# Kernel tuning notes

Measured on AMD Instinct MI355X. Metric: run time of the kernel, lower is better.

Reference implementation:

```python
import jax, jax.numpy as jnp
import numpy as np

N = 50000      # nodes
E = 800000     # edges (before self-loops)
F_IN = 128     # nfeat
H = 4          # heads
C = 64         # GAT out_channels per head
HID = 128      # GCN hidden
NCLASS = 10
NEG = 0.2      # leaky-relu negative slope (alpha)


def setup_inputs() -> dict:
    key = jax.random.key(0)
    ks = jax.random.split(key, 10)
    init = lambda k, shape, fan: jax.random.normal(k, shape, jnp.float32) / np.sqrt(fan).astype(np.float32)
    return {
        "x": jax.random.normal(ks[0], (N, F_IN), jnp.float32),
        "edge_attr": jax.random.normal(ks[1], (E, 8), jnp.float32),  # ignored (edge_dim=None in GATConv)
        "Wg": init(ks[2], (F_IN, H * C), F_IN),
        "att_src": init(ks[3], (H, C), C),
        "att_dst": init(ks[4], (H, C), C),
        "bg": jnp.zeros((H * C,), jnp.float32),
        "Wc": init(ks[5], (H * C, HID), H * C),
        "bc": jnp.zeros((HID,), jnp.float32),
        "Wl": init(ks[6], (HID, NCLASS), HID),
        "bl": jnp.zeros((NCLASS,), jnp.float32),
        "edge_index": jax.random.randint(ks[7], (2, E), 0, N, dtype=jnp.int64),
    }


def reference(x, edge_attr, Wg, att_src, att_dst, bg, Wc, bc, Wl, bl, edge_index):
    del edge_attr  # GATConv with edge_dim=None ignores edge_attr
    loop = jnp.arange(N, dtype=edge_index.dtype)
    src = jnp.concatenate([edge_index[0], loop])  # message sources j (add_self_loops=True)
    dst = jnp.concatenate([edge_index[1], loop])  # message targets i

    # ---- GATConv (concat=True) ----
    h = (x @ Wg).reshape(N, H, C)                     # [N,H,C]
    a_s = jnp.einsum('nhc,hc->nh', h, att_src)        # [N,H]
    a_d = jnp.einsum('nhc,hc->nh', h, att_dst)
    e = a_s[src] + a_d[dst]                           # [E2,H]
    e = jnp.where(e > 0, e, NEG * e)                  # leaky_relu
    m = jax.ops.segment_max(e, dst, num_segments=N)   # segment softmax over incoming edges
    ex = jnp.exp(e - m[dst])
    denom = jax.ops.segment_sum(ex, dst, num_segments=N)
    alpha = ex / denom[dst]                           # [E2,H]
    agg = jax.ops.segment_sum(alpha[:, :, None] * h[src], dst, num_segments=N)  # [N,H,C]
    xg = jax.nn.elu(agg.reshape(N, H * C) + bg)

    # ---- GCNConv (sym-normalized SpMM with self-loops) ----
    deg = jax.ops.segment_sum(jnp.ones_like(dst, dtype=jnp.float32), dst, num_segments=N)
    dinv = jnp.where(deg > 0, 1.0 / jnp.sqrt(deg), 0.0)
    norm = dinv[src] * dinv[dst]                      # [E2]
    xw = xg @ Wc                                      # [N,HID]
    xc = jax.ops.segment_sum(norm[:, None] * xw[src], dst, num_segments=N) + bc
    xc = jax.nn.relu(xc)

    # ---- classifier head ----
    logits = xc @ Wl + bl                             # [N,NCLASS]
    return jax.nn.log_softmax(logits, axis=1)
```

## Files before the change

kernel.cpp:

```cpp
#include <hip/hip_runtime.h>
#include <hip/hip_fp16.h>
#include <math.h>

#define NN 50000
#define EE 800000
#define E2 (EE + NN)
#define FIN 128
#define HC 256
#define HID 128
#define NCLS 10
#define NEG 0.2f
#define NB2 196
#define NBLK 256
#define WPART ((E2 + NBLK - 1) / NBLK)

typedef _Float16 f16x8 __attribute__((ext_vector_type(8)));
typedef float f32x4 __attribute__((ext_vector_type(4)));

#define FMA_MIX_LO(acc, u, w) \
    asm("v_fma_mix_f32 %0, %1, %2, %0 op_sel:[0,0,0] op_sel_hi:[1,0,0]" \
        : "+v"(acc) : "v"(u), "v"(w))
#define FMA_MIX_HI(acc, u, w) \
    asm("v_fma_mix_f32 %0, %1, %2, %0 op_sel:[1,0,0] op_sel_hi:[1,0,0]" \
        : "+v"(acc) : "v"(u), "v"(w))

__device__ inline uint pack2h(float a, float b) {
    return (uint)__half_as_ushort(__float2half(a)) |
           ((uint)__half_as_ushort(__float2half(b)) << 16);
}

__global__ __launch_bounds__(256) void prep_kernel(const float* __restrict__ Wg,
                                                   const float* __restrict__ Wc,
                                                   const float* __restrict__ att_s,
                                                   const float* __restrict__ att_d,
                                                   ushort* __restrict__ wgt,
                                                   ushort* __restrict__ wct,
                                                   float4* __restrict__ vs,
                                                   float4* __restrict__ vd) {
    int i = blockIdx.x * 256 + threadIdx.x;
    if (i < HC * FIN) {
        int c = i & 255, k = i >> 8;
        wgt[c * FIN + k] = __half_as_ushort(__float2half(Wg[i]));
        int c2 = i & 127, k2 = i >> 7;
        wct[c2 * HC + k2] = __half_as_ushort(__float2half(Wc[i]));
    }
    if (blockIdx.x == 0 && threadIdx.x < FIN) {
        int k = threadIdx.x;
        float s[4] = {0.f, 0.f, 0.f, 0.f}, d[4] = {0.f, 0.f, 0.f, 0.f};
        for (int h = 0; h < 4; ++h)
            for (int c = 0; c < 64; ++c) {
                float wv = Wg[k * HC + h * 64 + c];
                s[h] += wv * att_s[h * 64 + c];
                d[h] += wv * att_d[h * 64 + c];
            }
        vs[k] = make_float4(s[0], s[1], s[2], s[3]);
        vd[k] = make_float4(d[0], d[1], d[2], d[3]);
    }
}

__global__ __launch_bounds__(256) void prep_x(const float* __restrict__ x,
                                              const float4* __restrict__ vs,
                                              const float4* __restrict__ vd,
                                              ushort* __restrict__ x_half,
                                              float* __restrict__ a_s,
                                              float* __restrict__ a_d) {
    const int node = blockIdx.x * 4 + (threadIdx.x >> 6);
    const int lane = threadIdx.x & 63;
    if (node >= NN) return;
    float2 xv = ((const float2*)(x + (size_t)node * FIN))[lane];
    ((uint*)x_half)[(size_t)node * 64 + lane] = pack2h(xv.x, xv.y);
    float4 v0 = vs[2 * lane], v1 = vs[2 * lane + 1];
    float4 d0 = vd[2 * lane], d1 = vd[2 * lane + 1];
    float ps0 = xv.x * v0.x + xv.y * v1.x;
    float ps1 = xv.x * v0.y + xv.y * v1.y;
    float ps2 = xv.x * v0.z + xv.y * v1.z;
    float ps3 = xv.x * v0.w + xv.y * v1.w;
    float pd0 = xv.x * d0.x + xv.y * d1.x;
    float pd1 = xv.x * d0.y + xv.y * d1.y;
    float pd2 = xv.x * d0.z + xv.y * d1.z;
    float pd3 = xv.x * d0.w + xv.y * d1.w;
#pragma unroll
    for (int m = 32; m >= 1; m >>= 1) {
        ps0 += __shfl_xor(ps0, m, 64); ps1 += __shfl_xor(ps1, m, 64);
        ps2 += __shfl_xor(ps2, m, 64); ps3 += __shfl_xor(ps3, m, 64);
        pd0 += __shfl_xor(pd0, m, 64); pd1 += __shfl_xor(pd1, m, 64);
        pd2 += __shfl_xor(pd2, m, 64); pd3 += __shfl_xor(pd3, m, 64);
    }
    if (lane == 0) {
        ((float4*)a_s)[node] = make_float4(ps0, ps1, ps2, ps3);
        ((float4*)a_d)[node] = make_float4(pd0, pd1, pd2, pd3);
    }
}

__global__ __launch_bounds__(256) void hist_coarse(const int* __restrict__ ei,
                                                   uint* __restrict__ blockhist) {
    __shared__ uint h[NB2];
    for (int i = threadIdx.x; i < NB2; i += 256) h[i] = 0;
    __syncthreads();
    int e0 = blockIdx.x * WPART, e1 = min(E2, e0 + WPART);
    for (int e = e0 + threadIdx.x; e < e1; e += 256) {
        int dst = (e < EE) ? ei[EE + e] : e - EE;
        atomicAdd(&h[dst >> 8], 1u);
    }
    __syncthreads();
    for (int i = threadIdx.x; i < NB2; i += 256) blockhist[i * NBLK + blockIdx.x] = h[i];
}

__global__ __launch_bounds__(256) void scan_blocks(const uint* __restrict__ blockhist,
                                                   uint* __restrict__ blockoff,
                                                   uint* __restrict__ total) {
    __shared__ uint sh[256];
    int b = blockIdx.x, t = threadIdx.x;
    uint v = blockhist[b * NBLK + t];
    sh[t] = v;
    __syncthreads();
#pragma unroll
    for (int off = 1; off < 256; off <<= 1) {
        uint y = (t >= off) ? sh[t - off] : 0;
        __syncthreads();
        sh[t] += y;
        __syncthreads();
    }
    blockoff[b * NBLK + t] = sh[t] - v;
    if (t == 255) total[b] = sh[255];
}

__global__ __launch_bounds__(256) void scan_buckets(const uint* __restrict__ total,
                                                    uint* __restrict__ bucket_base) {
    __shared__ uint sh[256];
    int t = threadIdx.x;
    uint v = (t < NB2) ? total[t] : 0;
    sh[t] = v;
    __syncthreads();
#pragma unroll
    for (int off = 1; off < 256; off <<= 1) {
        uint y = (t >= off) ? sh[t - off] : 0;
        __syncthreads();
        sh[t] += y;
        __syncthreads();
    }
    if (t < NB2) bucket_base[t] = sh[t] - v;
    if (t == NB2 - 1) bucket_base[NB2] = sh[t];
}

__global__ __launch_bounds__(256) void reorder_kernel(const int* __restrict__ ei,
                                                      const uint* __restrict__ blockoff,
                                                      const uint* __restrict__ bucket_base,
                                                      uint* __restrict__ ebuf) {
    __shared__ uint cur[NB2];
    for (int i = threadIdx.x; i < NB2; i += 256)
        cur[i] = bucket_base[i] + blockoff[i * NBLK + blockIdx.x];
    __syncthreads();
    int e0 = blockIdx.x * WPART, e1 = min(E2, e0 + WPART);
    for (int e = e0 + threadIdx.x; e < e1; e += 256) {
        int src, dst;
        if (e < EE) { src = ei[e]; dst = ei[EE + e]; }
        else        { src = dst = e - EE; }
        uint p = atomicAdd(&cur[dst >> 8], 1u);
        ebuf[p] = (uint)src | ((uint)(dst & 255) << 16);
    }
}

__global__ __launch_bounds__(256) void bucket_csr(const uint* __restrict__ ebuf,
                                                  const uint* __restrict__ bucket_base,
                                                  int* __restrict__ row_start,
                                                  float* __restrict__ dinv,
                                                  ushort* __restrict__ csr_src) {
    __shared__ uint ldeg[256], lcur[256], sh[256];
    const int b = blockIdx.x, t = threadIdx.x;
    const uint base = bucket_base[b], end = bucket_base[b + 1];
    ldeg[t] = 0;
    __syncthreads();
    for (uint i = base + t; i < end; i += 256) atomicAdd(&ldeg[ebuf[i] >> 16], 1u);
    __syncthreads();
    uint v = ldeg[t];
    sh[t] = v;
    __syncthreads();
#pragma unroll
    for (int off = 1; off < 256; off <<= 1) {
        uint y = (t >= off) ? sh[t - off] : 0;
        __syncthreads();
        sh[t] += y;
        __syncthreads();
    }
    uint lscan = sh[t] - v;
    int node = b * 256 + t;
    if (node < NN) {
        row_start[node] = (int)(base + lscan);
        dinv[node] = rsqrtf((float)v);
    }
    lcur[t] = base + lscan;
    __syncthreads();
    for (uint i = base + t; i < end; i += 256) {
        uint pk = ebuf[i];
        uint p = atomicAdd(&lcur[pk >> 16], 1u);
        csr_src[p] = (ushort)(pk & 0xFFFFu);
    }
    if (b == 0 && t == 0) row_start[NN] = E2;
}

__global__ __launch_bounds__(256) void gat_x(const ushort* __restrict__ x_half,
                                             const float* __restrict__ a_s,
                                             const float* __restrict__ a_d,
                                             const int* __restrict__ row_start,
                                             const ushort* __restrict__ csr_src,
                                             ushort* __restrict__ y) {
    __shared__ int    lds_off[4][64];
    __shared__ float4 lds_ex[4][64];
    const int wid  = threadIdx.x >> 6;
    const int lane = threadIdx.x & 63;
    const int node = blockIdx.x * 4 + wid;
    if (node >= NN) return;
    const int s0 = row_start[node], s1 = row_start[node + 1];
    const float4 ad = ((const float4*)a_d)[node];

    float den0 = 0.f, den1 = 0.f, den2 = 0.f, den3 = 0.f;
    float a00=0.f,a01=0.f,a10=0.f,a11=0.f,a20=0.f,a21=0.f,a30=0.f,a31=0.f;
    const char* xbase = (const char*)x_half;
    const uint lane4 = (uint)lane * 4;

#define GAT_BODY(J)                                                \
    {                                                              \
        int off = lds_off[wid][J];                                 \
        float4 ex = lds_ex[wid][J];                                \
        uint u = *(const uint*)(xbase + ((uint)off + lane4));      \
        FMA_MIX_LO(a00, u, ex.x); FMA_MIX_HI(a01, u, ex.x);        \
        FMA_MIX_LO(a10, u, ex.y); FMA_MIX_HI(a11, u, ex.y);        \
        FMA_MIX_LO(a20, u, ex.z); FMA_MIX_HI(a21, u, ex.z);        \
        FMA_MIX_LO(a30, u, ex.w); FMA_MIX_HI(a31, u, ex.w);        \
    }

    for (int e = s0; e < s1; e += 64) {
        const int m = min(64, s1 - e);
        if (lane < m) {
            int src = (int)csr_src[e + lane];
            float4 as = ((const float4*)a_s)[src];
            float v0 = as.x + ad.x; v0 = v0 > 0.f ? v0 : NEG * v0;
            float v1 = as.y + ad.y; v1 = v1 > 0.f ? v1 : NEG * v1;
            float v2 = as.z + ad.z; v2 = v2 > 0.f ? v2 : NEG * v2;
            float v3 = as.w + ad.w; v3 = v3 > 0.f ? v3 : NEG * v3;
            float e0 = __expf(v0); den0 += e0;
            float e1 = __expf(v1); den1 += e1;
            float e2 = __expf(v2); den2 += e2;
            float e3 = __expf(v3); den3 += e3;
            lds_off[wid][lane] = src * 256;
            lds_ex[wid][lane]  = make_float4(e0, e1, e2, e3);
        }
        asm volatile("s_waitcnt lgkmcnt(0)" ::: "memory");
        int j = 0;
        for (; j + 8 <= m; j += 8) {
            GAT_BODY(j);     GAT_BODY(j + 1); GAT_BODY(j + 2); GAT_BODY(j + 3);
            GAT_BODY(j + 4); GAT_BODY(j + 5); GAT_BODY(j + 6); GAT_BODY(j + 7);
        }
        for (; j < m; ++j) GAT_BODY(j);
        asm volatile("" ::: "memory");
    }
#undef GAT_BODY
#pragma unroll
    for (int m = 32; m >= 1; m >>= 1) {
        den0 += __shfl_xor(den0, m, 64);
        den1 += __shfl_xor(den1, m, 64);
        den2 += __shfl_xor(den2, m, 64);
        den3 += __shfl_xor(den3, m, 64);
    }
    float r0 = 1.f / den0, r1 = 1.f / den1, r2 = 1.f / den2, r3 = 1.f / den3;
    uint* yrow = (uint*)y + (size_t)node * 256;
    yrow[0 * 64 + lane] = pack2h(a00 * r0, a01 * r0);
    yrow[1 * 64 + lane] = pack2h(a10 * r1, a11 * r1);
    yrow[2 * 64 + lane] = pack2h(a20 * r2, a21 * r2);
    yrow[3 * 64 + lane] = pack2h(a30 * r3, a31 * r3);
}

__global__ __launch_bounds__(256) void proj_mfma(const ushort* __restrict__ y,
                                                 const ushort* __restrict__ wgt,
                                                 const float* __restrict__ bg,
                                                 ushort* __restrict__ xg) {
    __shared__ ushort hs[16][264];
    const int t = threadIdx.x;
    const int w  = t >> 6;
    const int l  = t & 63;
    const int lr = l & 15;
    const int lg = l >> 4;
    const int rr = t >> 4;
    const int rc = (t & 15) * 8;

    f16x8 bf[4][4];
#pragma unroll
    for (int ct = 0; ct < 4; ++ct)
#pragma unroll
        for (int ks = 0; ks < 4; ++ks)
            bf[ct][ks] = *(const f16x8*)(wgt + (size_t)(64 * w + 16 * ct + lr) * FIN + ks * 32 + 8 * lg);

    float bgv[4];
#pragma unroll
    for (int ct = 0; ct < 4; ++ct) bgv[ct] = bg[64 * w + 16 * ct + lr];

    for (int rt = blockIdx.x; rt < 3125; rt += gridDim.x) {
        const int r0 = rt * 16;
        f32x4 acc[4];
#pragma unroll
        for (int ct = 0; ct < 4; ++ct) acc[ct] = (f32x4){0.f, 0.f, 0.f, 0.f};

#pragma unroll
        for (int ks = 0; ks < 4; ++ks) {
            f16x8 af = *(const f16x8*)(y + (size_t)(r0 + lr) * 512 + w * 128 + ks * 32 + 8 * lg);
#pragma unroll
            for (int ct = 0; ct < 4; ++ct)
                acc[ct] = __builtin_amdgcn_mfma_f32_16x16x32_f16(af, bf[ct][ks], acc[ct], 0, 0, 0);
        }
#pragma unroll
        for (int j = 0; j < 4; ++j) {
#pragma unroll
            for (int ct = 0; ct < 4; ++ct) {
                float o = acc[ct][j] + bgv[ct];
                o = o > 0.f ? o : __expf(o) - 1.f;
                hs[4 * lg + j][64 * w + 16 * ct + lr] = __half_as_ushort(__float2half(o));
            }
        }
        __syncthreads();
        *(uint4*)(xg + (size_t)(r0 + rr) * HC + rc)       = *(const uint4*)&hs[rr][rc];
        *(uint4*)(xg + (size_t)(r0 + rr) * HC + rc + 128) = *(const uint4*)&hs[rr][rc + 128];
        __syncthreads();
    }
}

__global__ __launch_bounds__(256) void gemm2_mfma(const ushort* __restrict__ xg,
                                                  const ushort* __restrict__ wct,
                                                  ushort* __restrict__ xw) {
    __shared__ ushort hs[16][136];
    const int t = threadIdx.x;
    const int w  = t >> 6;
    const int l  = t & 63;
    const int lr = l & 15;
    const int lg = l >> 4;
    const int rr = t >> 4;
    const int rc = (t & 15) * 8;

    f16x8 bf[2][8];
#pragma unroll
    for (int ct = 0; ct < 2; ++ct)
#pragma unroll
        for (int ks = 0; ks < 8; ++ks)
            bf[ct][ks] = *(const f16x8*)(wct + (size_t)(32 * w + 16 * ct + lr) * HC + ks * 32 + 8 * lg);

    for (int rt = blockIdx.x; rt < 3125; rt += gridDim.x) {
        const int r0 = rt * 16;
        f32x4 acc[2];
        acc[0] = (f32x4){0.f, 0.f, 0.f, 0.f};
        acc[1] = (f32x4){0.f, 0.f, 0.f, 0.f};
#pragma unroll
        for (int ks = 0; ks < 8; ++ks) {
            f16x8 af = *(const f16x8*)(xg + (size_t)(r0 + lr) * HC + ks * 32 + 8 * lg);
            acc[0] = __builtin_amdgcn_mfma_f32_16x16x32_f16(af, bf[0][ks], acc[0], 0, 0, 0);
            acc[1] = __builtin_amdgcn_mfma_f32_16x16x32_f16(af, bf[1][ks], acc[1], 0, 0, 0);
        }
#pragma unroll
        for (int j = 0; j < 4; ++j) {
#pragma unroll
            for (int ct = 0; ct < 2; ++ct)
                hs[4 * lg + j][32 * w + 16 * ct + lr] = __half_as_ushort(__float2half(acc[ct][j]));
        }
        __syncthreads();
        *(uint4*)(xw + (size_t)(r0 + rr) * HID + rc) = *(const uint4*)&hs[rr][rc];
        __syncthreads();
    }
}

__global__ __launch_bounds__(256) void gcn_head(const ushort* __restrict__ xw_half,
                                                const int* __restrict__ row_start,
                                                const ushort* __restrict__ csr_src,
                                                const float* __restrict__ dinv,
                                                const float* __restrict__ bc,
                                                const float* __restrict__ Wl,
                                                const float* __restrict__ bl,
                                                float* __restrict__ out) {
    __shared__ int2 lds_ow[4][64];
    const int wid  = threadIdx.x >> 6;
    const int lane = threadIdx.x & 63;
    const int node = blockIdx.x * 4 + wid;
    if (node >= NN) return;
    const int s0 = row_start[node], s1 = row_start[node + 1];
    const float di = dinv[node];
    float ax = 0.f, ay = 0.f;
    const char* xwbase = (const char*)xw_half;
    const uint lane4 = (uint)lane * 4;

#define GCN_BODY(OW)                                            \
    {                                                           \
        uint v = *(const uint*)(xwbase + ((uint)(OW).x + lane4)); \
        float ww = __int_as_float((OW).y);                      \
        FMA_MIX_LO(ax, v, ww); FMA_MIX_HI(ay, v, ww);           \
    }

    for (int e = s0; e < s1; e += 64) {
        const int m = min(64, s1 - e);
        if (lane < m) {
            int s = (int)csr_src[e + lane];
            lds_ow[wid][lane] = make_int2(s * 256, __float_as_int(dinv[s] * di));
        }
        asm volatile("s_waitcnt lgkmcnt(0)" ::: "memory");
        int j = 0;
        for (; j + 8 <= m; j += 8) {
            int2 ow0 = lds_ow[wid][j];
            int2 ow1 = lds_ow[wid][j + 1];
            int2 ow2 = lds_ow[wid][j + 2];
            int2 ow3 = lds_ow[wid][j + 3];
            int2 ow4 = lds_ow[wid][j + 4];
            int2 ow5 = lds_ow[wid][j + 5];
            int2 ow6 = lds_ow[wid][j + 6];
            int2 ow7 = lds_ow[wid][j + 7];
            GCN_BODY(ow0); GCN_BODY(ow1); GCN_BODY(ow2); GCN_BODY(ow3);
            GCN_BODY(ow4); GCN_BODY(ow5); GCN_BODY(ow6); GCN_BODY(ow7);
        }
        for (; j + 4 <= m; j += 4) {
            int2 ow0 = lds_ow[wid][j];
            int2 ow1 = lds_ow[wid][j + 1];
            int2 ow2 = lds_ow[wid][j + 2];
            int2 ow3 = lds_ow[wid][j + 3];
            GCN_BODY(ow0); GCN_BODY(ow1); GCN_BODY(ow2); GCN_BODY(ow3);
        }
        for (; j < m; ++j) {
            int2 ow = lds_ow[wid][j];
            GCN_BODY(ow);
        }
        asm volatile("" ::: "memory");
    }
#undef GCN_BODY
    float2 b = ((const float2*)bc)[lane];
    float o0 = ax + b.x; o0 = o0 > 0.f ? o0 : 0.f;
    float o1 = ay + b.y; o1 = o1 > 0.f ? o1 : 0.f;

    float p[NCLS];
#pragma unroll
    for (int j = 0; j < NCLS; ++j)
        p[j] = o0 * Wl[(2 * lane) * NCLS + j] + o1 * Wl[(2 * lane + 1) * NCLS + j];
#pragma unroll
    for (int m = 32; m >= 1; m >>= 1) {
#pragma unroll
        for (int j = 0; j < NCLS; ++j) p[j] += __shfl_xor(p[j], m, 64);
    }
#pragma unroll
    for (int j = 0; j < NCLS; ++j) p[j] += bl[j];
    float mx = p[0];
#pragma unroll
    for (int j = 1; j < NCLS; ++j) mx = fmaxf(mx, p[j]);
    float s = 0.f;
#pragma unroll
    for (int j = 0; j < NCLS; ++j) s += __expf(p[j] - mx);
    float ls = __logf(s);
    if (lane == 0) {
#pragma unroll
        for (int j = 0; j < NCLS; ++j) out[(size_t)node * NCLS + j] = p[j] - mx - ls;
    }
}

extern "C" void kernel_launch(void* const* d_in, const int* in_sizes, int n_in,
                              void* d_out, int out_size, void* d_ws, size_t ws_size,
                              hipStream_t stream) {
    const float* x       = (const float*)d_in[0];
    const float* Wg      = (const float*)d_in[2];
    const float* att_src = (const float*)d_in[3];
    const float* att_dst = (const float*)d_in[4];
    const float* bg      = (const float*)d_in[5];
    const float* Wc      = (const float*)d_in[6];
    const float* bc      = (const float*)d_in[7];
    const float* Wl      = (const float*)d_in[8];
    const float* bl      = (const float*)d_in[9];
    const int*   ei      = (const int*)d_in[10];
    float* out = (float*)d_out;

    char* p = (char*)d_ws;
    auto alloc = [&](size_t bytes) -> void* {
        void* r = (void*)p;
        p += (bytes + 255) & ~(size_t)255;
        return r;
    };
    ushort* x_half    = (ushort*)alloc((size_t)NN * FIN * 2);
    ushort* y         = (ushort*)alloc((size_t)NN * 512 * 2);
    ushort* xg_half   = (ushort*)alloc((size_t)NN * HC * 2);
    float*  a_s       = (float*)alloc((size_t)NN * 4 * 4);
    float*  a_d       = (float*)alloc((size_t)NN * 4 * 4);
    float*  dinv      = (float*)alloc((size_t)NN * 4);
    int*    row_start = (int*)alloc((size_t)(NN + 1) * 4);
    ushort* csr_src   = (ushort*)alloc((size_t)E2 * 2);
    uint*   ebuf      = (uint*)alloc((size_t)E2 * 4);
    uint*   blockhist = (uint*)alloc((size_t)NB2 * NBLK * 4);
    uint*   blockoff  = (uint*)alloc((size_t)NB2 * NBLK * 4);
    uint*   total     = (uint*)alloc(256 * 4);
    uint*   bucket_base = (uint*)alloc((NB2 + 1) * 4);
    ushort* wgt       = (ushort*)alloc((size_t)HC * FIN * 2);
    ushort* wct       = (ushort*)alloc((size_t)HID * HC * 2);
    float4* vs        = (float4*)alloc(FIN * 16);
    float4* vd        = (float4*)alloc(FIN * 16);
    ushort* xw_half   = x_half;

    prep_kernel<<<128, 256, 0, stream>>>(Wg, Wc, att_src, att_dst, wgt, wct, vs, vd);
    prep_x<<<(NN + 3) / 4, 256, 0, stream>>>(x, vs, vd, x_half, a_s, a_d);

    hist_coarse<<<NBLK, 256, 0, stream>>>(ei, blockhist);
    scan_blocks<<<NB2, 256, 0, stream>>>(blockhist, blockoff, total);
    scan_buckets<<<1, 256, 0, stream>>>(total, bucket_base);
    reorder_kernel<<<NBLK, 256, 0, stream>>>(ei, blockoff, bucket_base, ebuf);
    bucket_csr<<<NB2, 256, 0, stream>>>(ebuf, bucket_base, row_start, dinv, csr_src);

    gat_x<<<(NN + 3) / 4, 256, 0, stream>>>(x_half, a_s, a_d, row_start, csr_src, y);
    proj_mfma<<<1250, 256, 0, stream>>>(y, wgt, bg, xg_half);
    gemm2_mfma<<<1250, 256, 0, stream>>>(xg_half, wct, xw_half);
    gcn_head<<<(NN + 3) / 4, 256, 0, stream>>>(xw_half, row_start, csr_src, dinv, bc, Wl, bl, out);
}
```

Baseline: 204.6 us.

## Fuse GAT aggregation with both MFMA projections and fold bucket scan into consumers

Merges the GAT neighbour aggregation, the Wg projection with ELU, and the Wc GEMM into a single kernel that keeps 16-row tiles in LDS. This removes the global round-trips of the intermediate y (NN×512 half) and xg (NN×256 half) buffers and two launches. The single-block bucket scan kernel is also removed, and each reorder/csr block recomputes the 196-entry prefix itself. In exchange, each block reloads the weight fragments once per 16 rows instead of once per persistent block, and the larger LDS footprint may lower occupancy in the gather phase.

```diff
diff --git a/kernel.cpp b/kernel.cpp
--- a/kernel.cpp
+++ b/kernel.cpp
@@ -125,9 +125,12 @@
     if (t == 255) total[b] = sh[255];
 }
 
-__global__ __launch_bounds__(256) void scan_buckets(const uint* __restrict__ total,
-                                                    uint* __restrict__ bucket_base) {
+__global__ __launch_bounds__(256) void reorder_kernel(const int* __restrict__ ei,
+                                                      const uint* __restrict__ blockoff,
+                                                      const uint* __restrict__ total,
+                                                      uint* __restrict__ ebuf) {
     __shared__ uint sh[256];
+    __shared__ uint cur[NB2];
     int t = threadIdx.x;
     uint v = (t < NB2) ? total[t] : 0;
     sh[t] = v;
@@ -139,20 +142,10 @@
         sh[t] += y;
         __syncthreads();
     }
-    if (t < NB2) bucket_base[t] = sh[t] - v;
-    if (t == NB2 - 1) bucket_base[NB2] = sh[t];
-}
-
-__global__ __launch_bounds__(256) void reorder_kernel(const int* __restrict__ ei,
-                                                      const uint* __restrict__ blockoff,
-                                                      const uint* __restrict__ bucket_base,
-                                                      uint* __restrict__ ebuf) {
-    __shared__ uint cur[NB2];
-    for (int i = threadIdx.x; i < NB2; i += 256)
-        cur[i] = bucket_base[i] + blockoff[i * NBLK + blockIdx.x];
+    if (t < NB2) cur[t] = (sh[t] - v) + blockoff[t * NBLK + blockIdx.x];
     __syncthreads();
     int e0 = blockIdx.x * WPART, e1 = min(E2, e0 + WPART);
-    for (int e = e0 + threadIdx.x; e < e1; e += 256) {
+    for (int e = e0 + t; e < e1; e += 256) {
         int src, dst;
         if (e < EE) { src = ei[e]; dst = ei[EE + e]; }
         else        { src = dst = e - EE; }
@@ -162,18 +155,14 @@
 }
 
 __global__ __launch_bounds__(256) void bucket_csr(const uint* __restrict__ ebuf,
-                                                  const uint* __restrict__ bucket_base,
+                                                  const uint* __restrict__ total,
                                                   int* __restrict__ row_start,
                                                   float* __restrict__ dinv,
                                                   ushort* __restrict__ csr_src) {
     __shared__ uint ldeg[256], lcur[256], sh[256];
+    __shared__ uint sbe[2];
     const int b = blockIdx.x, t = threadIdx.x;
-    const uint base = bucket_base[b], end = bucket_base[b + 1];
-    ldeg[t] = 0;
-    __syncthreads();
-    for (uint i = base + t; i < end; i += 256) atomicAdd(&ldeg[ebuf[i] >> 16], 1u);
-    __syncthreads();
-    uint v = ldeg[t];
+    uint v = (t < NB2) ? total[t] : 0;
     sh[t] = v;
     __syncthreads();
 #pragma unroll
@@ -183,11 +172,27 @@
         sh[t] += y;
         __syncthreads();
     }
-    uint lscan = sh[t] - v;
+    if (t == b) { sbe[0] = sh[t] - v; sbe[1] = sh[t]; }
+    ldeg[t] = 0;
+    __syncthreads();
+    const uint base = sbe[0], end = sbe[1];
+    for (uint i = base + t; i < end; i += 256) atomicAdd(&ldeg[ebuf[i] >> 16], 1u);
+    __syncthreads();
+    uint dv = ldeg[t];
+    sh[t] = dv;
+    __syncthreads();
+#pragma unroll
+    for (int off = 1; off < 256; off <<= 1) {
+        uint y = (t >= off) ? sh[t - off] : 0;
+        __syncthreads();
+        sh[t] += y;
+        __syncthreads();
+    }
+    uint lscan = sh[t] - dv;
     int node = b * 256 + t;
     if (node < NN) {
         row_start[node] = (int)(base + lscan);
-        dinv[node] = rsqrtf((float)v);
+        dinv[node] = rsqrtf((float)dv);
     }
     lcur[t] = base + lscan;
     __syncthreads();
@@ -199,111 +204,109 @@
     if (b == 0 && t == 0) row_start[NN] = E2;
 }
 
-__global__ __launch_bounds__(256) void gat_x(const ushort* __restrict__ x_half,
-                                             const float* __restrict__ a_s,
-                                             const float* __restrict__ a_d,
-                                             const int* __restrict__ row_start,
-                                             const ushort* __restrict__ csr_src,
-                                             ushort* __restrict__ y) {
+__global__ __launch_bounds__(256) void gat_fused(const ushort* __restrict__ x_half,
+                                                 const float* __restrict__ a_s,
+                                                 const float* __restrict__ a_d,
+                                                 const int* __restrict__ row_start,
+                                                 const ushort* __restrict__ csr_src,
+                                                 const ushort* __restrict__ wgt,
+                                                 const float* __restrict__ bg,
+                                                 const ushort* __restrict__ wct,
+                                                 ushort* __restrict__ xw) {
+    __shared__ ushort yt[16][520];
+    __shared__ ushort xt[16][264];
+    __shared__ ushort xt2[16][136];
     __shared__ int    lds_off[4][64];
     __shared__ float4 lds_ex[4][64];
-    const int wid  = threadIdx.x >> 6;
-    const int lane = threadIdx.x & 63;
-    const int node = blockIdx.x * 4 + wid;
-    if (node >= NN) return;
-    const int s0 = row_start[node], s1 = row_start[node + 1];
-    const float4 ad = ((const float4*)a_d)[node];
-
-    float den0 = 0.f, den1 = 0.f, den2 = 0.f, den3 = 0.f;
-    float a00=0.f,a01=0.f,a10=0.f,a11=0.f,a20=0.f,a21=0.f,a30=0.f,a31=0.f;
+
+    const int t = threadIdx.x;
+    const int w = t >> 6;
+    const int lane = t & 63;
+    const int lr = lane & 15;
+    const int lg = lane >> 4;
+    const int rowbase = blockIdx.x * 16;
+
     const char* xbase = (const char*)x_half;
     const uint lane4 = (uint)lane * 4;
 
+    for (int i = 0; i < 4; ++i) {
+        const int nl = 4 * w + i;
+        const int node = rowbase + nl;
+        const int s0 = row_start[node], s1 = row_start[node + 1];
+        const float4 ad = ((const float4*)a_d)[node];
+
+        float den0 = 0.f, den1 = 0.f, den2 = 0.f, den3 = 0.f;
+        float a00=0.f,a01=0.f,a10=0.f,a11=0.f,a20=0.f,a21=0.f,a30=0.f,a31=0.f;
+
 #define GAT_BODY(J)                                                \
     {                                                              \
-        int off = lds_off[wid][J];                                 \
-        float4 ex = lds_ex[wid][J];                                \
+        int off = lds_off[w][J];                                   \
+        float4 ex = lds_ex[w][J];                                  \
         uint u = *(const uint*)(xbase + ((uint)off + lane4));      \
         FMA_MIX_LO(a00, u, ex.x); FMA_MIX_HI(a01, u, ex.x);        \
         FMA_MIX_LO(a10, u, ex.y); FMA_MIX_HI(a11, u, ex.y);        \
         FMA_MIX_LO(a20, u, ex.z); FMA_MIX_HI(a21, u, ex.z);        \
         FMA_MIX_LO(a30, u, ex.w); FMA_MIX_HI(a31, u, ex.w);        \
     }
-
-    for (int e = s0; e < s1; e += 64) {
-        const int m = min(64, s1 - e);
-        if (lane < m) {
-            int src = (int)csr_src[e + lane];
-            float4 as = ((const float4*)a_s)[src];
-            float v0 = as.x + ad.x; v0 = v0 > 0.f ? v0 : NEG * v0;
-            float v1 = as.y + ad.y; v1 = v1 > 0.f ? v1 : NEG * v1;
-            float v2 = as.z + ad.z; v2 = v2 > 0.f ? v2 : NEG * v2;
-            float v3 = as.w + ad.w; v3 = v3 > 0.f ? v3 : NEG * v3;
-            float e0 = __expf(v0); den0 += e0;
-            float e1 = __expf(v1); den1 += e1;
-            float e2 = __expf(v2); den2 += e2;
-            float e3 = __expf(v3); den3 += e3;
-            lds_off[wid][lane] = src * 256;
-            lds_ex[wid][lane]  = make_float4(e0, e1, e2, e3);
-        }
-        asm volatile("s_waitcnt lgkmcnt(0)" ::: "memory");
-        int j = 0;
-        for (; j + 8 <= m; j += 8) {
-            GAT_BODY(j);     GAT_BODY(j + 1); GAT_BODY(j + 2); GAT_BODY(j + 3);
-            GAT_BODY(j + 4); GAT_BODY(j + 5); GAT_BODY(j + 6); GAT_BODY(j + 7);
-        }
-        for (; j < m; ++j) GAT_BODY(j);
-        asm volatile("" ::: "memory");
-    }
+        for (int e = s0; e < s1; e += 64) {
+            const int m = min(64, s1 - e);
+            if (lane < m) {
+                int src = (int)csr_src[e + lane];
+                float4 as = ((const float4*)a_s)[src];
+                float v0 = as.x + ad.x; v0 = v0 > 0.f ? v0 : NEG * v0;
+                float v1 = as.y + ad.y; v1 = v1 > 0.f ? v1 : NEG * v1;
+                float v2 = as.z + ad.z; v2 = v2 > 0.f ? v2 : NEG * v2;
+                float v3 = as.w + ad.w; v3 = v3 > 0.f ? v3 : NEG * v3;
+                float e0 = __expf(v0); den0 += e0;
+                float e1 = __expf(v1); den1 += e1;
+                float e2 = __expf(v2); den2 += e2;
+                float e3 = __expf(v3); den3 += e3;
+                lds_off[w][lane] = src * 256;
+                lds_ex[w][lane]  = make_float4(e0, e1, e2, e3);
+            }
+            asm volatile("s_waitcnt lgkmcnt(0)" ::: "memory");
+            int j = 0;
+            for (; j + 8 <= m; j += 8) {
+                GAT_BODY(j);     GAT_BODY(j + 1); GAT_BODY(j + 2); GAT_BODY(j + 3);
+                GAT_BODY(j + 4); GAT_BODY(j + 5); GAT_BODY(j + 6); GAT_BODY(j + 7);
+            }
+            for (; j < m; ++j) GAT_BODY(j);
+            asm volatile("" ::: "memory");
+        }
 #undef GAT_BODY
 #pragma unroll
-    for (int m = 32; m >= 1; m >>= 1) {
-        den0 += __shfl_xor(den0, m, 64);
-        den1 += __shfl_xor(den1, m, 64);
-        den2 += __shfl_xor(den2, m, 64);
-        den3 += __shfl_xor(den3, m, 64);
-    }
-    float r0 = 1.f / den0, r1 = 1.f / den1, r2 = 1.f / den2, r3 = 1.f / den3;
-    uint* yrow = (uint*)y + (size_t)node * 256;
-    yrow[0 * 64 + lane] = pack2h(a00 * r0, a01 * r0);
-    yrow[1 * 64 + lane] = pack2h(a10 * r1, a11 * r1);
-    yrow[2 * 64 + lane] = pack2h(a20 * r2, a21 * r2);
-    yrow[3 * 64 + lane] = pack2h(a30 * r3, a31 * r3);
-}
-
-__global__ __launch_bounds__(256) void proj_mfma(const ushort* __restrict__ y,
-                                                 const ushort* __restrict__ wgt,
-                                                 const float* __restrict__ bg,
-                                                 ushort* __restrict__ xg) {
-    __shared__ ushort hs[16][264];
-    const int t = threadIdx.x;
-    const int w  = t >> 6;
-    const int l  = t & 63;
-    const int lr = l & 15;
-    const int lg = l >> 4;
-    const int rr = t >> 4;
-    const int rc = (t & 15) * 8;
-
-    f16x8 bf[4][4];
-#pragma unroll
-    for (int ct = 0; ct < 4; ++ct)
-#pragma unroll
-        for (int ks = 0; ks < 4; ++ks)
-            bf[ct][ks] = *(const f16x8*)(wgt + (size_t)(64 * w + 16 * ct + lr) * FIN + ks * 32 + 8 * lg);
-
-    float bgv[4];
-#pragma unroll
-    for (int ct = 0; ct < 4; ++ct) bgv[ct] = bg[64 * w + 16 * ct + lr];
-
-    for (int rt = blockIdx.x; rt < 3125; rt += gridDim.x) {
-        const int r0 = rt * 16;
+        for (int m = 32; m >= 1; m >>= 1) {
+            den0 += __shfl_xor(den0, m, 64);
+            den1 += __shfl_xor(den1, m, 64);
+            den2 += __shfl_xor(den2, m, 64);
+            den3 += __shfl_xor(den3, m, 64);
+        }
+        float r0 = 1.f / den0, r1 = 1.f / den1, r2 = 1.f / den2, r3 = 1.f / den3;
+        uint* yu = (uint*)&yt[nl][0];
+        yu[0 * 64 + lane] = pack2h(a00 * r0, a01 * r0);
+        yu[1 * 64 + lane] = pack2h(a10 * r1, a11 * r1);
+        yu[2 * 64 + lane] = pack2h(a20 * r2, a21 * r2);
+        yu[3 * 64 + lane] = pack2h(a30 * r3, a31 * r3);
+    }
+    __syncthreads();
+
+    {
+        f16x8 bf[4][4];
+#pragma unroll
+        for (int ct = 0; ct < 4; ++ct)
+#pragma unroll
+            for (int ks = 0; ks < 4; ++ks)
+                bf[ct][ks] = *(const f16x8*)(wgt + (size_t)(64 * w + 16 * ct + lr) * FIN + ks * 32 + 8 * lg);
+        float bgv[4];
+#pragma unroll
+        for (int ct = 0; ct < 4; ++ct) bgv[ct] = bg[64 * w + 16 * ct + lr];
+
         f32x4 acc[4];
 #pragma unroll
         for (int ct = 0; ct < 4; ++ct) acc[ct] = (f32x4){0.f, 0.f, 0.f, 0.f};
-
 #pragma unroll
         for (int ks = 0; ks < 4; ++ks) {
-            f16x8 af = *(const f16x8*)(y + (size_t)(r0 + lr) * 512 + w * 128 + ks * 32 + 8 * lg);
+            f16x8 af = *(const f16x8*)&yt[lr][w * 128 + ks * 32 + 8 * lg];
 #pragma unroll
             for (int ct = 0; ct < 4; ++ct)
                 acc[ct] = __builtin_amdgcn_mfma_f32_16x16x32_f16(af, bf[ct][ks], acc[ct], 0, 0, 0);
@@ -314,55 +317,42 @@
             for (int ct = 0; ct < 4; ++ct) {
                 float o = acc[ct][j] + bgv[ct];
                 o = o > 0.f ? o : __expf(o) - 1.f;
-                hs[4 * lg + j][64 * w + 16 * ct + lr] = __half_as_ushort(__float2half(o));
+                xt[4 * lg + j][64 * w + 16 * ct + lr] = __half_as_ushort(__float2half(o));
             }
         }
-        __syncthreads();
-        *(uint4*)(xg + (size_t)(r0 + rr) * HC + rc)       = *(const uint4*)&hs[rr][rc];
-        *(uint4*)(xg + (size_t)(r0 + rr) * HC + rc + 128) = *(const uint4*)&hs[rr][rc + 128];
-        __syncthreads();
-    }
-}
-
-__global__ __launch_bounds__(256) void gemm2_mfma(const ushort* __restrict__ xg,
-                                                  const ushort* __restrict__ wct,
-                                                  ushort* __restrict__ xw) {
-    __shared__ ushort hs[16][136];
-    const int t = threadIdx.x;
-    const int w  = t >> 6;
-    const int l  = t & 63;
-    const int lr = l & 15;
-    const int lg = l >> 4;
-    const int rr = t >> 4;
-    const int rc = (t & 15) * 8;
-
-    f16x8 bf[2][8];
-#pragma unroll
-    for (int ct = 0; ct < 2; ++ct)
-#pragma unroll
-        for (int ks = 0; ks < 8; ++ks)
-            bf[ct][ks] = *(const f16x8*)(wct + (size_t)(32 * w + 16 * ct + lr) * HC + ks * 32 + 8 * lg);
-
-    for (int rt = blockIdx.x; rt < 3125; rt += gridDim.x) {
-        const int r0 = rt * 16;
-        f32x4 acc[2];
-        acc[0] = (f32x4){0.f, 0.f, 0.f, 0.f};
-        acc[1] = (f32x4){0.f, 0.f, 0.f, 0.f};
+    }
+    __syncthreads();
+
+    {
+        f16x8 bf2[2][8];
+#pragma unroll
+        for (int ct = 0; ct < 2; ++ct)
+#pragma unroll
+            for (int ks = 0; ks < 8; ++ks)
+                bf2[ct][ks] = *(const f16x8*)(wct + (size_t)(32 * w + 16 * ct + lr) * HC + ks * 32 + 8 * lg);
+
+        f32x4 acc2[2];
+        acc2[0] = (f32x4){0.f, 0.f, 0.f, 0.f};
+        acc2[1] = (f32x4){0.f, 0.f, 0.f, 0.f};
 #pragma unroll
         for (int ks = 0; ks < 8; ++ks) {
-            f16x8 af = *(const f16x8*)(xg + (size_t)(r0 + lr) * HC + ks * 32 + 8 * lg);
-            acc[0] = __builtin_amdgcn_mfma_f32_16x16x32_f16(af, bf[0][ks], acc[0], 0, 0, 0);
-            acc[1] = __builtin_amdgcn_mfma_f32_16x16x32_f16(af, bf[1][ks], acc[1], 0, 0, 0);
+            f16x8 af = *(const f16x8*)&xt[lr][ks * 32 + 8 * lg];
+            acc2[0] = __builtin_amdgcn_mfma_f32_16x16x32_f16(af, bf2[0][ks], acc2[0], 0, 0, 0);
+            acc2[1] = __builtin_amdgcn_mfma_f32_16x16x32_f16(af, bf2[1][ks], acc2[1], 0, 0, 0);
         }
 #pragma unroll
         for (int j = 0; j < 4; ++j) {
 #pragma unroll
             for (int ct = 0; ct < 2; ++ct)
-                hs[4 * lg + j][32 * w + 16 * ct + lr] = __half_as_ushort(__float2half(acc[ct][j]));
-        }
-        __syncthreads();
-        *(uint4*)(xw + (size_t)(r0 + rr) * HID + rc) = *(const uint4*)&hs[rr][rc];
-        __syncthreads();
+                xt2[4 * lg + j][32 * w + 16 * ct + lr] = __half_as_ushort(__float2half(acc2[ct][j]));
+        }
+    }
+    __syncthreads();
+
+    {
+        const int rr = t >> 4;
+        const int rc = (t & 15) * 8;
+        *(uint4*)(xw + (size_t)(rowbase + rr) * HID + rc) = *(const uint4*)&xt2[rr][rc];
     }
 }
 
@@ -476,8 +466,7 @@
         return r;
     };
     ushort* x_half    = (ushort*)alloc((size_t)NN * FIN * 2);
-    ushort* y         = (ushort*)alloc((size_t)NN * 512 * 2);
-    ushort* xg_half   = (ushort*)alloc((size_t)NN * HC * 2);
+    ushort* xw_half   = (ushort*)alloc((size_t)NN * HID * 2);
     float*  a_s       = (float*)alloc((size_t)NN * 4 * 4);
     float*  a_d       = (float*)alloc((size_t)NN * 4 * 4);
     float*  dinv      = (float*)alloc((size_t)NN * 4);
@@ -487,24 +476,20 @@
     uint*   blockhist = (uint*)alloc((size_t)NB2 * NBLK * 4);
     uint*   blockoff  = (uint*)alloc((size_t)NB2 * NBLK * 4);
     uint*   total     = (uint*)alloc(256 * 4);
-    uint*   bucket_base = (uint*)alloc((NB2 + 1) * 4);
     ushort* wgt       = (ushort*)alloc((size_t)HC * FIN * 2);
     ushort* wct       = (ushort*)alloc((size_t)HID * HC * 2);
     float4* vs        = (float4*)alloc(FIN * 16);
     float4* vd        = (float4*)alloc(FIN * 16);
-    ushort* xw_half   = x_half;
 
     prep_kernel<<<128, 256, 0, stream>>>(Wg, Wc, att_src, att_dst, wgt, wct, vs, vd);
     prep_x<<<(NN + 3) / 4, 256, 0, stream>>>(x, vs, vd, x_half, a_s, a_d);
 
     hist_coarse<<<NBLK, 256, 0, stream>>>(ei, blockhist);
     scan_blocks<<<NB2, 256, 0, stream>>>(blockhist, blockoff, total);
-    scan_buckets<<<1, 256, 0, stream>>>(total, bucket_base);
-    reorder_kernel<<<NBLK, 256, 0, stream>>>(ei, blockoff, bucket_base, ebuf);
-    bucket_csr<<<NB2, 256, 0, stream>>>(ebuf, bucket_base, row_start, dinv, csr_src);
-
-    gat_x<<<(NN + 3) / 4, 256, 0, stream>>>(x_half, a_s, a_d, row_start, csr_src, y);
-    proj_mfma<<<1250, 256, 0, stream>>>(y, wgt, bg, xg_half);
-    gemm2_mfma<<<1250, 256, 0, stream>>>(xg_half, wct, xw_half);
+    reorder_kernel<<<NBLK, 256, 0, stream>>>(ei, blockoff, total, ebuf);
+    bucket_csr<<<NB2, 256, 0, stream>>>(ebuf, total, row_start, dinv, csr_src);
+
+    gat_fused<<<NN / 16, 256, 0, stream>>>(x_half, a_s, a_d, row_start, csr_src,
+                                           wgt, bg, wct, xw_half);
     gcn_head<<<(NN + 3) / 4, 256, 0, stream>>>(xw_half, row_start, csr_src, dinv, bc, Wl, bl, out);
 }
```

New measurement: 217.1 us. 6.1% more time.
